# Kernel tuning notes

Hardware: AMD Instinct MI355X
Metric: run time of the kernel (lower is better)

Reference implementation:

```python
import jax, jax.numpy as jnp
import numpy as np

S = 3072      # total packed tokens
D = 1536      # hidden_size
H = 12        # num_heads
HD = D // H   # head_dim = 128
NSEQ = 4      # number of packed sequences (images)


def rotate_half(x):
    x1 = x[..., : x.shape[-1] // 2]
    x2 = x[..., x.shape[-1] // 2 :]
    return jnp.concatenate((-x2, x1), axis=-1)


def setup_inputs() -> dict:
    key = jax.random.key(0)
    k1, k2, k3 = jax.random.split(key, 3)
    hidden_states = jax.random.normal(k1, (S, D), jnp.float32)
    # 4 equal-length packed sequences
    cu_seqlens = (jnp.arange(NSEQ + 1, dtype=jnp.int32) * (S // NSEQ))
    # RoPE cos/sin per token, period within each packed sequence
    pos = (jnp.arange(S) % (S // NSEQ)).astype(jnp.float32)
    inv_freq = 1.0 / (10000.0 ** (jnp.arange(0, HD // 2, dtype=jnp.float32) / (HD // 2)))
    freqs = pos[:, None] * inv_freq[None, :]          # [S, HD//2]
    emb = jnp.concatenate([freqs, freqs], axis=-1)    # [S, HD]
    cos, sin = jnp.cos(emb), jnp.sin(emb)
    qkv_w = jax.random.normal(k2, (3 * D, D), jnp.float32) * (D ** -0.5)
    qkv_b = jnp.zeros((3 * D,), jnp.float32)
    proj_w = jax.random.normal(k3, (D, D), jnp.float32) * (D ** -0.5)
    return {
        "hidden_states": hidden_states,
        "cos": cos,
        "sin": sin,
        "qkv_w": qkv_w,
        "qkv_b": qkv_b,
        "proj_w": proj_w,
        "cu_seqlens": cu_seqlens,
    }


def reference(hidden_states, cos, sin, qkv_w, qkv_b, proj_w, cu_seqlens):
    s_len, dim = hidden_states.shape
    # fused QKV projection -> [S, 3, H, HD]
    qkv = (hidden_states @ qkv_w.T + qkv_b).reshape(s_len, 3, H, HD)
    q, k, v = qkv[:, 0], qkv[:, 1], qkv[:, 2]         # each [S, H, HD]
    # inline RoPE (fp32, broadcast over heads)
    c = cos[:, None, :].astype(jnp.float32)
    s = sin[:, None, :].astype(jnp.float32)
    qf, kf = q.astype(jnp.float32), k.astype(jnp.float32)
    q = (qf * c + rotate_half(qf) * s).astype(q.dtype)
    k = (kf * c + rotate_half(kf) * s).astype(k.dtype)
    # block-diagonal (varlen) mask from cu_seqlens
    seg = jnp.searchsorted(cu_seqlens, jnp.arange(s_len), side="right")  # [S]
    same_seq = seg[:, None] == seg[None, :]                              # [S, S]
    bias = jnp.where(same_seq, 0.0, -jnp.inf).astype(jnp.float32)
    scaling = HD ** -0.5
    # scores [H, S, S]
    scores = jnp.einsum("shd,thd->hst", q, k) * scaling + bias[None]
    probs = jax.nn.softmax(scores.astype(jnp.float32), axis=-1).astype(q.dtype)
    attn = jnp.einsum("hst,thd->shd", probs, v).reshape(s_len, dim)
    return attn @ proj_w.T
```

## Files before the change

### kernel.cpp

```cpp
#include <hip/hip_runtime.h>
#include <stdint.h>

#define S_LEN 3072
#define DIM   1536
#define NH    12
#define HD    128
#define QKV_N 4608

typedef unsigned short u16;
typedef unsigned int   u32;
typedef __bf16 bf16x8 __attribute__((ext_vector_type(8)));
typedef float  f32x4  __attribute__((ext_vector_type(4)));
typedef u16    u16x8  __attribute__((ext_vector_type(8)));
typedef u16    u16x4  __attribute__((ext_vector_type(4)));
typedef u32    u32x4  __attribute__((ext_vector_type(4)));

#define AS1 __attribute__((address_space(1)))
#define AS3 __attribute__((address_space(3)))
#define GLL16(g, l) __builtin_amdgcn_global_load_lds((AS1 void*)(g), (AS3 void*)(l), 16, 0, 0)

__device__ __forceinline__ u16 f2bf(float f) {
  unsigned u = __float_as_uint(f);
  u = (u + 0x7fffu + ((u >> 16) & 1u)) >> 16;
  return (u16)u;
}
__device__ __forceinline__ float bf2f(u16 b) {
  return __uint_as_float(((unsigned)b) << 16);
}

__global__ __launch_bounds__(256) void cvt_bf16_3(const float* __restrict__ in0, u16* __restrict__ out0, int n0,
                                                  const float* __restrict__ in1, u16* __restrict__ out1, int n1,
                                                  const float* __restrict__ in2, u16* __restrict__ out2, int n2) {
  int total = n0 + n1 + n2;
  int stride = gridDim.x * blockDim.x;
  for (int i = blockIdx.x * blockDim.x + threadIdx.x; i < total; i += stride) {
    const float* src; u16* dst; int j;
    if (i < n0)           { src = in0; dst = out0; j = i; }
    else if (i < n0 + n1) { src = in1; dst = out1; j = i - n0; }
    else                  { src = in2; dst = out2; j = i - n0 - n1; }
    float4 v = ((const float4*)src)[j];
    ushort4 o;
    o.x = f2bf(v.x); o.y = f2bf(v.y); o.z = f2bf(v.z); o.w = f2bf(v.w);
    ((ushort4*)dst)[j] = o;
  }
}

__global__ __launch_bounds__(512, 2) void gemm_qkvf(const u16* __restrict__ A,
                                                    const u16* __restrict__ B,
                                                    const float* __restrict__ bias,
                                                    const float* __restrict__ cosb,
                                                    const float* __restrict__ sinb,
                                                    u16* __restrict__ Qp,
                                                    u16* __restrict__ Kp,
                                                    u16* __restrict__ Vt,
                                                    int M, int N, int K) {
  __shared__ __attribute__((aligned(16))) u16 lds[8 * 8192];

  const int t = threadIdx.x;
  const int l = t & 63;
  const int w = t >> 6;
  const int wm = w >> 2;
  const int wn = w & 3;
  const int lr = l & 15;
  const int lc = l >> 4;

  const int nbx = N >> 8;
  const int nwg = gridDim.x;
  const int q = nwg >> 3, r = nwg & 7;
  const int xcd = blockIdx.x & 7, rest = blockIdx.x >> 3;
  const int wgid = (xcd < r ? xcd * (q + 1) : r * (q + 1) + (xcd - r) * q) + rest;
  const int m0 = (wgid / nbx) * 256;
  const int n0 = (wgid % nbx) * 256;

  const int nk = K >> 6;

  f32x4 acc[8][4];
  #pragma unroll
  for (int i = 0; i < 8; ++i)
    #pragma unroll
    for (int j = 0; j < 4; ++j) acc[i][j] = f32x4{0.f, 0.f, 0.f, 0.f};

  auto frag2 = [&](const u16* region, int row, int ch) {
    int L = row >> 1;
    int slot = ((ch + ((row & 1) << 2)) ^ L) & 7;
    return *(const bf16x8*)(region + L * 64 + slot * 8);
  };
  auto stage_half = [&](int buf, int ks, int ab, int kt) {
    const u16* base = ab ? B : A;
    const int x0 = ab ? n0 : m0;
    u16* dst = lds + (((buf << 2) | (ks << 1) | ab) * 8192);
    #pragma unroll
    for (int i = 0; i < 2; ++i) {
      int C = t + i * 512;
      int L = C >> 3, s = C & 7;
      int u = s ^ (L & 7);
      int row = 2 * L + (u >> 2), ch = u & 3;
      const u16* src = base + (size_t)(x0 + row) * K + kt * 64 + ks * 32 + ch * 8;
      GLL16(src, dst + C * 8);
    }
  };

  stage_half(0, 0, 0, 0); stage_half(0, 0, 1, 0);
  stage_half(0, 1, 0, 0); stage_half(0, 1, 1, 0);
  if (nk > 1) { stage_half(1, 0, 0, 1); stage_half(1, 0, 1, 1); }
  asm volatile("s_waitcnt vmcnt(4)" ::: "memory");
  __builtin_amdgcn_s_barrier();

  for (int kt = 0; kt < nk; ++kt) {
    const int buf = kt & 1, nbuf = buf ^ 1;
    const bool st1 = (kt + 1 < nk);
    const bool st2 = (kt + 2 < nk);

    const u16* A0 = lds + (((buf << 2) | 0) * 8192);
    const u16* B0 = lds + (((buf << 2) | 1) * 8192);
    const u16* A1 = lds + (((buf << 2) | 2) * 8192);
    const u16* B1 = lds + (((buf << 2) | 3) * 8192);

    bf16x8 bfrag[4], afr[4];

    #pragma unroll
    for (int ni = 0; ni < 4; ++ni) bfrag[ni] = frag2(B0, wn * 64 + ni * 16 + lr, lc);
    #pragma unroll
    for (int mi = 0; mi < 4; ++mi) afr[mi] = frag2(A0, wm * 128 + mi * 16 + lr, lc);
    if (st1) stage_half(nbuf, 1, 0, kt + 1);
    __builtin_amdgcn_s_barrier();
    __builtin_amdgcn_s_setprio(1);
    #pragma unroll
    for (int mi = 0; mi < 4; ++mi)
      #pragma unroll
      for (int ni = 0; ni < 4; ++ni)
        acc[mi][ni] = __builtin_amdgcn_mfma_f32_16x16x32_bf16(afr[mi], bfrag[ni],
                                                              acc[mi][ni], 0, 0, 0);
    __builtin_amdgcn_s_setprio(0);
    __builtin_amdgcn_s_barrier();

    #pragma unroll
    for (int mi = 0; mi < 4; ++mi) afr[mi] = frag2(A0, wm * 128 + 64 + mi * 16 + lr, lc);
    if (st1) stage_half(nbuf, 1, 1, kt + 1);
    __builtin_amdgcn_s_barrier();
    __builtin_amdgcn_s_setprio(1);
    #pragma unroll
    for (int mi = 0; mi < 4; ++mi)
      #pragma unroll
      for (int ni = 0; ni < 4; ++ni)
        acc[4 + mi][ni] = __builtin_amdgcn_mfma_f32_16x16x32_bf16(afr[mi], bfrag[ni],
                                                                  acc[4 + mi][ni], 0, 0, 0);
    __builtin_amdgcn_s_setprio(0);
    __builtin_amdgcn_s_barrier();

    #pragma unroll
    for (int ni = 0; ni < 4; ++ni) bfrag[ni] = frag2(B1, wn * 64 + ni * 16 + lr, lc);
    #pragma unroll
    for (int mi = 0; mi < 4; ++mi) afr[mi] = frag2(A1, wm * 128 + mi * 16 + lr, lc);
    if (st2) stage_half(buf, 0, 0, kt + 2);
    __builtin_amdgcn_s_barrier();
    __builtin_amdgcn_s_setprio(1);
    #pragma unroll
    for (int mi = 0; mi < 4; ++mi)
      #pragma unroll
      for (int ni = 0; ni < 4; ++ni)
        acc[mi][ni] = __builtin_amdgcn_mfma_f32_16x16x32_bf16(afr[mi], bfrag[ni],
                                                              acc[mi][ni], 0, 0, 0);
    __builtin_amdgcn_s_setprio(0);
    __builtin_amdgcn_s_barrier();

    #pragma unroll
    for (int mi = 0; mi < 4; ++mi) afr[mi] = frag2(A1, wm * 128 + 64 + mi * 16 + lr, lc);
    if (st2) {
      stage_half(buf, 0, 1, kt + 2);
      asm volatile("s_waitcnt vmcnt(4)" ::: "memory");
    } else if (st1) {
      asm volatile("s_waitcnt vmcnt(0)" ::: "memory");
    }
    __builtin_amdgcn_s_barrier();
    __builtin_amdgcn_s_setprio(1);
    #pragma unroll
    for (int mi = 0; mi < 4; ++mi)
      #pragma unroll
      for (int ni = 0; ni < 4; ++ni)
        acc[4 + mi][ni] = __builtin_amdgcn_mfma_f32_16x16x32_bf16(afr[mi], bfrag[ni],
                                                                  acc[4 + mi][ni], 0, 0, 0);
    __builtin_amdgcn_s_setprio(0);
    __builtin_amdgcn_s_barrier();
  }

  const int sec = n0 / DIM;
  const int h0 = (n0 % DIM) >> 7;

  {
    float bv[4];
    #pragma unroll
    for (int ni = 0; ni < 4; ++ni)
      bv[ni] = bias[n0 + wn * 64 + ni * 16 + lr];
    #pragma unroll
    for (int mi = 0; mi < 8; ++mi) {
      int rbase = wm * 128 + mi * 16 + lc * 4;
      int s4 = (rbase >> 3) & 15;
      #pragma unroll
      for (int ni = 0; ni < 4; ++ni) {
        int scol = (wn * 64 + ni * 16 + lr) ^ (s4 << 4);
        #pragma unroll
        for (int rr = 0; rr < 4; ++rr)
          lds[(rbase + rr) * 256 + scol] = f2bf(acc[mi][ni][rr] + bv[ni]);
      }
    }
  }
  __syncthreads();

  if (sec < 2) {
    u16* dst = sec ? Kp : Qp;
    const float sc = sec ? 1.f : (0.08838834764831845f * 1.4426950408889634f);
    #pragma unroll
    for (int i = 0; i < 16; ++i) {
      int id = i * 512 + t;
      int row = id >> 5, c16 = id & 31;
      int srow = m0 + row;
      int s4 = (row >> 3) & 15;
      int c8 = c16 * 8;
      u16x8 x  = *(const u16x8*)(lds + row * 256 + (c8 ^ (s4 << 4)));
      u16x8 xp = *(const u16x8*)(lds + row * 256 + ((c8 ^ 64) ^ (s4 << 4)));
      int h = h0 + (c8 >> 7);
      int d = c8 & 127;
      float cs[8], sn[8];
      *(float4*)(cs)     = *(const float4*)(cosb + (size_t)srow * HD + d);
      *(float4*)(cs + 4) = *(const float4*)(cosb + (size_t)srow * HD + d + 4);
      *(float4*)(sn)     = *(const float4*)(sinb + (size_t)srow * HD + d);
      *(float4*)(sn + 4) = *(const float4*)(sinb + (size_t)srow * HD + d + 4);
      const float sg = (d & 64) ? 1.f : -1.f;
      u16x8 o;
      #pragma unroll
      for (int j = 0; j < 8; ++j)
        o[j] = f2bf((bf2f(x[j]) * cs[j] + sg * bf2f(xp[j]) * sn[j]) * sc);
      *(u16x8*)(dst + ((size_t)h * S_LEN + srow) * HD + d) = o;
    }
  } else {
    #pragma unroll
    for (int i = 0; i < 16; ++i) {
      int id = i * 512 + t;
      int col = (((id >> 6) & 31) << 3) | ((id >> 3) & 7);
      int sch = (id & 7) | (((id >> 11) & 3) << 3);
      int h = h0 + (col >> 7), d = col & 127;
      int scol = col ^ ((sch & 15) << 4);
      u16x8 v;
      #pragma unroll
      for (int e = 0; e < 8; ++e)
        v[e] = lds[(sch * 8 + e) * 256 + scol];
      *(u16x8*)(Vt + ((size_t)h * HD + d) * S_LEN + m0 + sch * 8) = v;
    }
  }
}

__device__ __forceinline__ bf16x8 lds_frag(const u16* base, int row, int ch) {
  return *(const bf16x8*)(base + row * 64 + ((ch ^ row) & 7) * 8);
}

__global__ __launch_bounds__(256) void gemm_proj(const u16* __restrict__ A,
                                                 const u16* __restrict__ B,
                                                 float* __restrict__ Cout,
                                                 int M, int N, int K) {
  __shared__ __attribute__((aligned(16))) u16 smem[2 * 128 * 64];
  u16* Asm = smem;
  u16* Bsm = smem + 128 * 64;

  const int t = threadIdx.x;
  const int l = t & 63;
  const int w = t >> 6;
  const int wm = w >> 1, wn = w & 1;
  const int lr = l & 15;
  const int lq = l >> 4;

  const int nbx = N >> 7;
  const int nwg = gridDim.x;
  const int qc = nwg >> 3, rc = nwg & 7;
  const int xcd = blockIdx.x & 7, rest = blockIdx.x >> 3;
  const int wgid = (xcd < rc ? xcd * (qc + 1) : rc * (qc + 1) + (xcd - rc) * qc) + rest;
  const int m0 = (wgid / nbx) * 128;
  const int n0 = (wgid % nbx) * 128;

  f32x4 acc[4][4];
  #pragma unroll
  for (int i = 0; i < 4; ++i)
    #pragma unroll
    for (int j = 0; j < 4; ++j) acc[i][j] = f32x4{0.f, 0.f, 0.f, 0.f};

  for (int k0 = 0; k0 < K; k0 += 64) {
    __syncthreads();
    #pragma unroll
    for (int r4 = 0; r4 < 4; ++r4) {
      int C = t + r4 * 256;
      int row = C >> 3, ch = C & 7;
      int sch = (ch ^ row) & 7;
      GLL16(A + (size_t)(m0 + row) * K + k0 + sch * 8, Asm + (size_t)C * 8);
      GLL16(B + (size_t)(n0 + row) * K + k0 + sch * 8, Bsm + (size_t)C * 8);
    }
    __syncthreads();
    #pragma unroll
    for (int ks = 0; ks < 2; ++ks) {
      bf16x8 af[4], bfr[4];
      #pragma unroll
      for (int mi = 0; mi < 4; ++mi)
        af[mi] = lds_frag(Asm, wm * 64 + mi * 16 + lr, ks * 4 + lq);
      #pragma unroll
      for (int ni = 0; ni < 4; ++ni)
        bfr[ni] = lds_frag(Bsm, wn * 64 + ni * 16 + lr, ks * 4 + lq);
      #pragma unroll
      for (int mi = 0; mi < 4; ++mi)
        #pragma unroll
        for (int ni = 0; ni < 4; ++ni)
          acc[mi][ni] = __builtin_amdgcn_mfma_f32_16x16x32_bf16(af[mi], bfr[ni],
                                                                acc[mi][ni], 0, 0, 0);
    }
  }

  float* Cf = (float*)smem;
  #pragma unroll
  for (int p = 0; p < 2; ++p) {
    __syncthreads();
    if (wm == p) {
      #pragma unroll
      for (int mi = 0; mi < 4; ++mi)
        #pragma unroll
        for (int ni = 0; ni < 4; ++ni) {
          int colb = wn * 64 + ni * 16 + lr;
          #pragma unroll
          for (int rr = 0; rr < 4; ++rr) {
            int row = mi * 16 + lq * 4 + rr;
            int scol = colb ^ (((row >> 2) & 1) << 4);
            Cf[row * 128 + scol] = acc[mi][ni][rr];
          }
        }
    }
    __syncthreads();
    #pragma unroll
    for (int i = 0; i < 8; ++i) {
      int id = i * 256 + t;
      int row = id >> 5, c4 = id & 31;
      int scol = (c4 * 4) ^ (((row >> 2) & 1) << 4);
      float4 v = *(const float4*)(Cf + row * 128 + scol);
      *(float4*)(Cout + (size_t)(m0 + p * 64 + row) * N + n0 + c4 * 4) = v;
    }
  }
}

__global__ __launch_bounds__(256) void attn_fwd(const u16* __restrict__ Qp,
                                                const u16* __restrict__ Kp,
                                                const u16* __restrict__ Vt,
                                                const int* __restrict__ cu,
                                                u16* __restrict__ Obf) {
  __shared__ u16 K_lds[64 * 128];
  __shared__ u16 VT_lds[128 * 64];

  const int t = threadIdx.x;
  const int l = t & 63;
  const int lr = l & 15;
  const int lq = l >> 4;
  const int w = t >> 6;

  const int nwg = gridDim.x;
  const int qc = nwg >> 3, rc = nwg & 7;
  const int xcd = blockIdx.x & 7, rest = blockIdx.x >> 3;
  const int wgid = (xcd < rc ? xcd * (qc + 1) : rc * (qc + 1) + (xcd - rc) * qc) + rest;
  const int h = wgid / (S_LEN / 64);
  const int q0 = (wgid % (S_LEN / 64)) * 64;

  int cs = 0, ce = S_LEN;
  #pragma unroll
  for (int b = 0; b < 4; ++b) {
    int lo = cu[b], hi = cu[b + 1];
    if (q0 >= lo && q0 < hi) { cs = lo; ce = hi; }
  }

  const int qrow = q0 + w * 16 + lr;
  bf16x8 qf[4];
  const u16* qptr = Qp + ((size_t)h * S_LEN + qrow) * HD + lq * 8;
  #pragma unroll
  for (int ks = 0; ks < 4; ++ks) qf[ks] = *(const bf16x8*)(qptr + ks * 32);

  f32x4 acc_o[8];
  #pragma unroll
  for (int i = 0; i < 8; ++i) acc_o[i] = f32x4{0.f, 0.f, 0.f, 0.f};
  float m_run = -1e30f, l_run = 0.f;

  const int o0 = ((l & 16) << 1) | lr;
  const int o1 = o0 + 16;
  const int hisel = lq >> 1;

  for (int kv0 = cs; kv0 < ce; kv0 += 64) {
    __syncthreads();
    {
      const u16* kbase = Kp + ((size_t)h * S_LEN + kv0) * HD;
      #pragma unroll
      for (int r4 = 0; r4 < 4; ++r4) {
        int C = t + r4 * 256;
        int row = C >> 4, ch = C & 15;
        int sch = (ch & 8) | ((ch ^ row) & 7);
        GLL16(kbase + row * HD + sch * 8, K_lds + (size_t)C * 8);
      }
      const u16* vbase = Vt + (size_t)h * HD * S_LEN + kv0;
      #pragma unroll
      for (int r4 = 0; r4 < 4; ++r4) {
        int C = t + r4 * 256;
        int row = C >> 3, ch = C & 7;
        int sch = (ch ^ row) & 7;
        GLL16(vbase + (size_t)row * S_LEN + sch * 8, VT_lds + (size_t)C * 8);
      }
    }
    __syncthreads();

    f32x4 s_acc[4];
    __builtin_amdgcn_s_setprio(1);
    #pragma unroll
    for (int nf = 0; nf < 4; ++nf) {
      s_acc[nf] = f32x4{0.f, 0.f, 0.f, 0.f};
      int krow = nf * 16 + lr;
      #pragma unroll
      for (int ks = 0; ks < 4; ++ks) {
        int ch = ks * 4 + lq;
        int sch = (ch & 8) | ((ch ^ krow) & 7);
        bf16x8 kf = *(const bf16x8*)(K_lds + krow * 128 + sch * 8);
        s_acc[nf] = __builtin_amdgcn_mfma_f32_16x16x32_bf16(kf, qf[ks], s_acc[nf], 0, 0, 0);
      }
    }
    __builtin_amdgcn_s_setprio(0);

    float vmax = -1e30f;
    #pragma unroll
    for (int nf = 0; nf < 4; ++nf)
      #pragma unroll
      for (int r = 0; r < 4; ++r) vmax = fmaxf(vmax, s_acc[nf][r]);
    vmax = fmaxf(vmax, __shfl_xor(vmax, 16, 64));
    vmax = fmaxf(vmax, __shfl_xor(vmax, 32, 64));
    float mn = fmaxf(m_run, vmax);
    float alpha = __builtin_amdgcn_exp2f(m_run - mn);
    m_run = mn;
    float pv[4][4], sum = 0.f;
    #pragma unroll
    for (int nf = 0; nf < 4; ++nf)
      #pragma unroll
      for (int r = 0; r < 4; ++r) {
        float e = __builtin_amdgcn_exp2f(s_acc[nf][r] - mn);
        pv[nf][r] = e;
        sum += e;
      }
    sum += __shfl_xor(sum, 16, 64);
    sum += __shfl_xor(sum, 32, 64);
    l_run = l_run * alpha + sum;

    float alphaO[4];
    #pragma unroll
    for (int r = 0; r < 4; ++r) alphaO[r] = __shfl(alpha, lq * 20 + r, 64);
    #pragma unroll
    for (int onf = 0; onf < 8; ++onf)
      #pragma unroll
      for (int r = 0; r < 4; ++r) acc_o[onf][r] *= alphaO[r];

    u32 plo[4], phi[4];
    #pragma unroll
    for (int nf = 0; nf < 4; ++nf) {
      plo[nf] = (u32)f2bf(pv[nf][0]) | ((u32)f2bf(pv[nf][1]) << 16);
      phi[nf] = (u32)f2bf(pv[nf][2]) | ((u32)f2bf(pv[nf][3]) << 16);
    }

    #pragma unroll
    for (int ks = 0; ks < 2; ++ks) {
      u32 a0 = __shfl(plo[ks * 2], o0, 64), b0 = __shfl(plo[ks * 2 + 1], o0, 64);
      u32 a1 = __shfl(phi[ks * 2], o0, 64), b1 = __shfl(phi[ks * 2 + 1], o0, 64);
      u32 a2 = __shfl(plo[ks * 2], o1, 64), b2 = __shfl(plo[ks * 2 + 1], o1, 64);
      u32 a3 = __shfl(phi[ks * 2], o1, 64), b3 = __shfl(phi[ks * 2 + 1], o1, 64);
      u32x4 pau;
      pau[0] = hisel ? b0 : a0;
      pau[1] = hisel ? b1 : a1;
      pau[2] = hisel ? b2 : a2;
      pau[3] = hisel ? b3 : a3;
      bf16x8 pa = __builtin_bit_cast(bf16x8, pau);
      __builtin_amdgcn_s_setprio(1);
      #pragma unroll
      for (int onf = 0; onf < 8; ++onf) {
        int d = onf * 16 + lr;
        int ch = ks * 4 + lq;
        int sch = (ch ^ d) & 7;
        bf16x8 vf = *(const bf16x8*)(VT_lds + d * 64 + sch * 8);
        acc_o[onf] = __builtin_amdgcn_mfma_f32_16x16x32_bf16(pa, vf, acc_o[onf], 0, 0, 0);
      }
      __builtin_amdgcn_s_setprio(0);
    }
  }

  float invO[4];
  #pragma unroll
  for (int r = 0; r < 4; ++r) invO[r] = 1.f / __shfl(l_run, lq * 20 + r, 64);
  #pragma unroll
  for (int r = 0; r < 4; ++r) {
    int srow = q0 + w * 16 + (lq << 2) + r;
    u16* orow = Obf + (size_t)srow * DIM + h * HD + lr;
    #pragma unroll
    for (int onf = 0; onf < 8; ++onf) orow[onf * 16] = f2bf(acc_o[onf][r] * invO[r]);
  }
}

extern "C" void kernel_launch(void* const* d_in, const int* in_sizes, int n_in,
                              void* d_out, int out_size, void* d_ws, size_t ws_size,
                              hipStream_t stream) {
  const float* hidden = (const float*)d_in[0];
  const float* cosb   = (const float*)d_in[1];
  const float* sinb   = (const float*)d_in[2];
  const float* qkv_w  = (const float*)d_in[3];
  const float* qkv_b  = (const float*)d_in[4];
  const float* proj_w = (const float*)d_in[5];
  const int*   cu     = (const int*)d_in[6];

  u16* Hbf   = (u16*)d_ws;
  u16* Wqkv  = Hbf   + (size_t)S_LEN * DIM;
  u16* Wproj = Wqkv  + (size_t)QKV_N * DIM;
  u16* Qp    = Wproj + (size_t)DIM * DIM;
  u16* Kp    = Qp    + (size_t)NH * S_LEN * HD;
  u16* Vt    = Kp    + (size_t)NH * S_LEN * HD;
  u16* Abf   = Hbf;

  cvt_bf16_3<<<2048, 256, 0, stream>>>(hidden, Hbf, S_LEN * DIM / 4,
                                       qkv_w, Wqkv, QKV_N * DIM / 4,
                                       proj_w, Wproj, DIM * DIM / 4);

  gemm_qkvf<<<(S_LEN / 256) * (QKV_N / 256), 512, 0, stream>>>(
      Hbf, Wqkv, qkv_b, cosb, sinb, Qp, Kp, Vt, S_LEN, QKV_N, DIM);

  attn_fwd<<<(S_LEN / 64) * NH, 256, 0, stream>>>(Qp, Kp, Vt, cu, Abf);

  gemm_proj<<<(S_LEN / 128) * (DIM / 128), 256, 0, stream>>>(
      Abf, Wproj, (float*)d_out, S_LEN, DIM, DIM);
}
```

Before: 139.4 us.

## Halve QKV GEMM LDS footprint with K32 double buffering and two-pass epilogue

The QKV GEMM previously staged two 32-wide K slices per buffer (128 KB of LDS). It now stages one 32-wide slice per double-buffered stage (64 KB), so the main loop runs twice as many iterations with a full vmcnt(0) wait each time. The epilogue is split into two passes, each writing and reading 128 rows, so the 256x256 output tile fits in the smaller LDS. The aim is to let two 512-thread workgroups share a CU, as the launch bounds request. The cost is a shallower prefetch, more barriers per K step, and an extra epilogue barrier round.

```diff
diff --git a/kernel.cpp b/kernel.cpp
--- a/kernel.cpp
+++ b/kernel.cpp
@@ -54,7 +54,7 @@
                                                     u16* __restrict__ Kp,
                                                     u16* __restrict__ Vt,
                                                     int M, int N, int K) {
-  __shared__ __attribute__((aligned(16))) u16 lds[8 * 8192];
+  __shared__ __attribute__((aligned(16))) u16 lds[4 * 8192];
 
   const int t = threadIdx.x;
   const int l = t & 63;
@@ -72,7 +72,7 @@
   const int m0 = (wgid / nbx) * 256;
   const int n0 = (wgid % nbx) * 256;
 
-  const int nk = K >> 6;
+  const int nk = K >> 5;
 
   f32x4 acc[8][4];
   #pragma unroll
@@ -85,44 +85,38 @@
     int slot = ((ch + ((row & 1) << 2)) ^ L) & 7;
     return *(const bf16x8*)(region + L * 64 + slot * 8);
   };
-  auto stage_half = [&](int buf, int ks, int ab, int kt) {
+  auto stage_mat = [&](int buf, int ab, int kt) {
     const u16* base = ab ? B : A;
     const int x0 = ab ? n0 : m0;
-    u16* dst = lds + (((buf << 2) | (ks << 1) | ab) * 8192);
+    u16* dst = lds + (((buf << 1) | ab) * 8192);
     #pragma unroll
     for (int i = 0; i < 2; ++i) {
       int C = t + i * 512;
       int L = C >> 3, s = C & 7;
       int u = s ^ (L & 7);
       int row = 2 * L + (u >> 2), ch = u & 3;
-      const u16* src = base + (size_t)(x0 + row) * K + kt * 64 + ks * 32 + ch * 8;
+      const u16* src = base + (size_t)(x0 + row) * K + kt * 32 + ch * 8;
       GLL16(src, dst + C * 8);
     }
   };
 
-  stage_half(0, 0, 0, 0); stage_half(0, 0, 1, 0);
-  stage_half(0, 1, 0, 0); stage_half(0, 1, 1, 0);
-  if (nk > 1) { stage_half(1, 0, 0, 1); stage_half(1, 0, 1, 1); }
-  asm volatile("s_waitcnt vmcnt(4)" ::: "memory");
+  stage_mat(0, 0, 0); stage_mat(0, 1, 0);
+  asm volatile("s_waitcnt vmcnt(0)" ::: "memory");
   __builtin_amdgcn_s_barrier();
 
   for (int kt = 0; kt < nk; ++kt) {
     const int buf = kt & 1, nbuf = buf ^ 1;
-    const bool st1 = (kt + 1 < nk);
-    const bool st2 = (kt + 2 < nk);
-
-    const u16* A0 = lds + (((buf << 2) | 0) * 8192);
-    const u16* B0 = lds + (((buf << 2) | 1) * 8192);
-    const u16* A1 = lds + (((buf << 2) | 2) * 8192);
-    const u16* B1 = lds + (((buf << 2) | 3) * 8192);
+    const bool st = (kt + 1 < nk);
+    const u16* Ar = lds + (((buf << 1) | 0) * 8192);
+    const u16* Br = lds + (((buf << 1) | 1) * 8192);
 
     bf16x8 bfrag[4], afr[4];
 
     #pragma unroll
-    for (int ni = 0; ni < 4; ++ni) bfrag[ni] = frag2(B0, wn * 64 + ni * 16 + lr, lc);
-    #pragma unroll
-    for (int mi = 0; mi < 4; ++mi) afr[mi] = frag2(A0, wm * 128 + mi * 16 + lr, lc);
-    if (st1) stage_half(nbuf, 1, 0, kt + 1);
+    for (int ni = 0; ni < 4; ++ni) bfrag[ni] = frag2(Br, wn * 64 + ni * 16 + lr, lc);
+    #pragma unroll
+    for (int mi = 0; mi < 4; ++mi) afr[mi] = frag2(Ar, wm * 128 + mi * 16 + lr, lc);
+    if (st) stage_mat(nbuf, 0, kt + 1);
     __builtin_amdgcn_s_barrier();
     __builtin_amdgcn_s_setprio(1);
     #pragma unroll
@@ -135,8 +129,8 @@
     __builtin_amdgcn_s_barrier();
 
     #pragma unroll
-    for (int mi = 0; mi < 4; ++mi) afr[mi] = frag2(A0, wm * 128 + 64 + mi * 16 + lr, lc);
-    if (st1) stage_half(nbuf, 1, 1, kt + 1);
+    for (int mi = 0; mi < 4; ++mi) afr[mi] = frag2(Ar, wm * 128 + 64 + mi * 16 + lr, lc);
+    if (st) stage_mat(nbuf, 1, kt + 1);
     __builtin_amdgcn_s_barrier();
     __builtin_amdgcn_s_setprio(1);
     #pragma unroll
@@ -146,106 +140,77 @@
         acc[4 + mi][ni] = __builtin_amdgcn_mfma_f32_16x16x32_bf16(afr[mi], bfrag[ni],
                                                                   acc[4 + mi][ni], 0, 0, 0);
     __builtin_amdgcn_s_setprio(0);
-    __builtin_amdgcn_s_barrier();
-
-    #pragma unroll
-    for (int ni = 0; ni < 4; ++ni) bfrag[ni] = frag2(B1, wn * 64 + ni * 16 + lr, lc);
-    #pragma unroll
-    for (int mi = 0; mi < 4; ++mi) afr[mi] = frag2(A1, wm * 128 + mi * 16 + lr, lc);
-    if (st2) stage_half(buf, 0, 0, kt + 2);
-    __builtin_amdgcn_s_barrier();
-    __builtin_amdgcn_s_setprio(1);
-    #pragma unroll
-    for (int mi = 0; mi < 4; ++mi)
-      #pragma unroll
-      for (int ni = 0; ni < 4; ++ni)
-        acc[mi][ni] = __builtin_amdgcn_mfma_f32_16x16x32_bf16(afr[mi], bfrag[ni],
-                                                              acc[mi][ni], 0, 0, 0);
-    __builtin_amdgcn_s_setprio(0);
-    __builtin_amdgcn_s_barrier();
-
-    #pragma unroll
-    for (int mi = 0; mi < 4; ++mi) afr[mi] = frag2(A1, wm * 128 + 64 + mi * 16 + lr, lc);
-    if (st2) {
-      stage_half(buf, 0, 1, kt + 2);
-      asm volatile("s_waitcnt vmcnt(4)" ::: "memory");
-    } else if (st1) {
-      asm volatile("s_waitcnt vmcnt(0)" ::: "memory");
-    }
-    __builtin_amdgcn_s_barrier();
-    __builtin_amdgcn_s_setprio(1);
-    #pragma unroll
-    for (int mi = 0; mi < 4; ++mi)
-      #pragma unroll
-      for (int ni = 0; ni < 4; ++ni)
-        acc[4 + mi][ni] = __builtin_amdgcn_mfma_f32_16x16x32_bf16(afr[mi], bfrag[ni],
-                                                                  acc[4 + mi][ni], 0, 0, 0);
-    __builtin_amdgcn_s_setprio(0);
+    if (st) asm volatile("s_waitcnt vmcnt(0)" ::: "memory");
     __builtin_amdgcn_s_barrier();
   }
 
   const int sec = n0 / DIM;
   const int h0 = (n0 % DIM) >> 7;
 
-  {
-    float bv[4];
-    #pragma unroll
-    for (int ni = 0; ni < 4; ++ni)
-      bv[ni] = bias[n0 + wn * 64 + ni * 16 + lr];
-    #pragma unroll
-    for (int mi = 0; mi < 8; ++mi) {
-      int rbase = wm * 128 + mi * 16 + lc * 4;
-      int s4 = (rbase >> 3) & 15;
-      #pragma unroll
-      for (int ni = 0; ni < 4; ++ni) {
-        int scol = (wn * 64 + ni * 16 + lr) ^ (s4 << 4);
+  float bv[4];
+  #pragma unroll
+  for (int ni = 0; ni < 4; ++ni)
+    bv[ni] = bias[n0 + wn * 64 + ni * 16 + lr];
+
+  #pragma unroll
+  for (int p = 0; p < 2; ++p) {
+    __syncthreads();
+    if (wm == p) {
+      #pragma unroll
+      for (int mi = 0; mi < 8; ++mi) {
+        int rbase = mi * 16 + lc * 4;
+        int s4 = (rbase >> 3) & 15;
         #pragma unroll
-        for (int rr = 0; rr < 4; ++rr)
-          lds[(rbase + rr) * 256 + scol] = f2bf(acc[mi][ni][rr] + bv[ni]);
-      }
-    }
-  }
-  __syncthreads();
-
-  if (sec < 2) {
-    u16* dst = sec ? Kp : Qp;
-    const float sc = sec ? 1.f : (0.08838834764831845f * 1.4426950408889634f);
-    #pragma unroll
-    for (int i = 0; i < 16; ++i) {
-      int id = i * 512 + t;
-      int row = id >> 5, c16 = id & 31;
-      int srow = m0 + row;
-      int s4 = (row >> 3) & 15;
-      int c8 = c16 * 8;
-      u16x8 x  = *(const u16x8*)(lds + row * 256 + (c8 ^ (s4 << 4)));
-      u16x8 xp = *(const u16x8*)(lds + row * 256 + ((c8 ^ 64) ^ (s4 << 4)));
-      int h = h0 + (c8 >> 7);
-      int d = c8 & 127;
-      float cs[8], sn[8];
-      *(float4*)(cs)     = *(const float4*)(cosb + (size_t)srow * HD + d);
-      *(float4*)(cs + 4) = *(const float4*)(cosb + (size_t)srow * HD + d + 4);
-      *(float4*)(sn)     = *(const float4*)(sinb + (size_t)srow * HD + d);
-      *(float4*)(sn + 4) = *(const float4*)(sinb + (size_t)srow * HD + d + 4);
-      const float sg = (d & 64) ? 1.f : -1.f;
-      u16x8 o;
-      #pragma unroll
-      for (int j = 0; j < 8; ++j)
-        o[j] = f2bf((bf2f(x[j]) * cs[j] + sg * bf2f(xp[j]) * sn[j]) * sc);
-      *(u16x8*)(dst + ((size_t)h * S_LEN + srow) * HD + d) = o;
-    }
-  } else {
-    #pragma unroll
-    for (int i = 0; i < 16; ++i) {
-      int id = i * 512 + t;
-      int col = (((id >> 6) & 31) << 3) | ((id >> 3) & 7);
-      int sch = (id & 7) | (((id >> 11) & 3) << 3);
-      int h = h0 + (col >> 7), d = col & 127;
-      int scol = col ^ ((sch & 15) << 4);
-      u16x8 v;
-      #pragma unroll
-      for (int e = 0; e < 8; ++e)
-        v[e] = lds[(sch * 8 + e) * 256 + scol];
-      *(u16x8*)(Vt + ((size_t)h * HD + d) * S_LEN + m0 + sch * 8) = v;
+        for (int ni = 0; ni < 4; ++ni) {
+          int scol = (wn * 64 + ni * 16 + lr) ^ (s4 << 4);
+          #pragma unroll
+          for (int rr = 0; rr < 4; ++rr)
+            lds[(rbase + rr) * 256 + scol] = f2bf(acc[mi][ni][rr] + bv[ni]);
+        }
+      }
+    }
+    __syncthreads();
+
+    if (sec < 2) {
+      u16* dst = sec ? Kp : Qp;
+      const float sc = sec ? 1.f : (0.08838834764831845f * 1.4426950408889634f);
+      #pragma unroll
+      for (int i = 0; i < 8; ++i) {
+        int id = i * 512 + t;
+        int row = id >> 5, c16 = id & 31;
+        int srow = m0 + p * 128 + row;
+        int s4 = (row >> 3) & 15;
+        int c8 = c16 * 8;
+        u16x8 x  = *(const u16x8*)(lds + row * 256 + (c8 ^ (s4 << 4)));
+        u16x8 xp = *(const u16x8*)(lds + row * 256 + ((c8 ^ 64) ^ (s4 << 4)));
+        int h = h0 + (c8 >> 7);
+        int d = c8 & 127;
+        float cs[8], sn[8];
+        *(float4*)(cs)     = *(const float4*)(cosb + (size_t)srow * HD + d);
+        *(float4*)(cs + 4) = *(const float4*)(cosb + (size_t)srow * HD + d + 4);
+        *(float4*)(sn)     = *(const float4*)(sinb + (size_t)srow * HD + d);
+        *(float4*)(sn + 4) = *(const float4*)(sinb + (size_t)srow * HD + d + 4);
+        const float sg = (d & 64) ? 1.f : -1.f;
+        u16x8 o;
+        #pragma unroll
+        for (int j = 0; j < 8; ++j)
+          o[j] = f2bf((bf2f(x[j]) * cs[j] + sg * bf2f(xp[j]) * sn[j]) * sc);
+        *(u16x8*)(dst + ((size_t)h * S_LEN + srow) * HD + d) = o;
+      }
+    } else {
+      #pragma unroll
+      for (int i = 0; i < 8; ++i) {
+        int id = i * 512 + t;
+        int col = (((id >> 6) & 31) << 3) | ((id >> 3) & 7);
+        int schl = (id & 7) | (((id >> 11) & 1) << 3);
+        int h = h0 + (col >> 7), d = col & 127;
+        int scol = col ^ ((schl & 15) << 4);
+        u16x8 v;
+        #pragma unroll
+        for (int e = 0; e < 8; ++e)
+          v[e] = lds[(schl * 8 + e) * 256 + scol];
+        *(u16x8*)(Vt + ((size_t)h * HD + d) * S_LEN + m0 + p * 128 + schl * 8) = v;
+      }
     }
   }
 }
```

Measured after the change: 148.6 us (median of 2 runs). +6.6%, slower.
